# Kernel optimization log

Hardware: AMD Instinct MI355X
Metric: run time of the kernel (lower is better)

## Reference

```python
import jax, jax.numpy as jnp
import numpy as np

H = 1024  # hidden size


def lstm_layer(x, W_ih, W_hh, b_ih, b_hh):
    # x: [B, T, in] -> outputs [B, T, H]; torch gate order (i, f, g, o)
    xg = jnp.einsum('bti,gi->btg', x, W_ih) + (b_ih + b_hh)  # [B, T, 4H]
    xg = jnp.swapaxes(xg, 0, 1)  # [T, B, 4H] for scan over time
    B = x.shape[0]
    h0 = jnp.zeros((B, H), x.dtype)
    c0 = jnp.zeros((B, H), x.dtype)

    def step(carry, xg_t):
        h, c = carry
        g = xg_t + h @ W_hh.T  # [B, 4H]
        i, f, gc, o = jnp.split(g, 4, axis=-1)
        i = jax.nn.sigmoid(i)
        f = jax.nn.sigmoid(f)
        gc = jnp.tanh(gc)
        o = jax.nn.sigmoid(o)
        c = f * c + i * gc
        h = o * jnp.tanh(c)
        return (h, c), h

    (_, _), hs = jax.lax.scan(step, (h0, c0), xg)
    return jnp.swapaxes(hs, 0, 1)  # [B, T, H]


def setup_inputs() -> dict:
    key = jax.random.key(0)
    ks = jax.random.split(key, 11)
    s = 1.0 / np.sqrt(H)  # torch LSTM init scale
    return {
        'x': jax.random.normal(ks[0], (64, 512, 128), jnp.float32),
        'W_ih0': jax.random.normal(ks[1], (4 * H, 128), jnp.float32) * s,
        'W_hh0': jax.random.normal(ks[2], (4 * H, H), jnp.float32) * s,
        'b_ih0': jax.random.normal(ks[3], (4 * H,), jnp.float32) * s,
        'b_hh0': jax.random.normal(ks[4], (4 * H,), jnp.float32) * s,
        'W_ih1': jax.random.normal(ks[5], (4 * H, H), jnp.float32) * s,
        'W_hh1': jax.random.normal(ks[6], (4 * H, H), jnp.float32) * s,
        'b_ih1': jax.random.normal(ks[7], (4 * H,), jnp.float32) * s,
        'b_hh1': jax.random.normal(ks[8], (4 * H,), jnp.float32) * s,
        'fc_w': jax.random.normal(ks[9], (1, H), jnp.float32) * s,
        'fc_b': jax.random.normal(ks[10], (1,), jnp.float32) * s,
    }


def reference(x, W_ih0, W_hh0, b_ih0, b_hh0, W_ih1, W_hh1, b_ih1, b_hh1, fc_w, fc_b):
    h1 = lstm_layer(x, W_ih0, W_hh0, b_ih0, b_hh0)   # [B, T, H]
    h2 = lstm_layer(h1, W_ih1, W_hh1, b_ih1, b_hh1)  # [B, T, H]
    return h2[:, -1, :] @ fc_w.T + fc_b              # [B, 1]
```

## Files before the change

kernel.cpp:

```cpp
#include <hip/hip_runtime.h>
#include <math.h>

#define HDIM 1024
#define BDIM 64
#define TDIM 512
#define KIN  128
#define NBLK 256
#define NTHR 1024
#define FRAME (HDIM * BDIM)

typedef _Float16 f16;
typedef __attribute__((ext_vector_type(2))) _Float16 f16x2;
typedef __attribute__((ext_vector_type(8))) _Float16 f16x8;
typedef __attribute__((ext_vector_type(4))) float f32x4;

#define MFMA16(a, b, c) __builtin_amdgcn_mfma_f32_16x16x32_f16((a), (b), (c), 0, 0, 0)

__device__ __forceinline__ float sigm(float x) { return 1.0f / (1.0f + expf(-x)); }

__device__ __forceinline__ f16x8 ld_cg(const f16* p) {
    f16x8 r;
    asm volatile("global_load_dwordx4 %0, %1, off sc0 sc1"
                 : "=v"(r) : "v"(p) : "memory");
    return r;
}
#define VM_WAIT8(r0, r1, r2, r3, r4, r5, r6, r7)                         \
    asm volatile("s_waitcnt vmcnt(0)"                                    \
                 : "+v"(r0), "+v"(r1), "+v"(r2), "+v"(r3),               \
                   "+v"(r4), "+v"(r5), "+v"(r6), "+v"(r7))

__device__ __forceinline__ void st_cg8(f16* p, uint2 v) {
    asm volatile("global_store_dwordx2 %0, %1, off sc0 sc1"
                 :: "v"(p), "v"(v) : "memory");
}
#define VM_DRAIN() asm volatile("s_waitcnt vmcnt(0)" ::: "memory")

__device__ __forceinline__ void bar_add(unsigned* base, int slot) {
    __hip_atomic_fetch_add(base + slot * 32, 1u, __ATOMIC_RELAXED,
                           __HIP_MEMORY_SCOPE_AGENT);
}
__device__ __forceinline__ void bar_wait(unsigned* base, unsigned target) {
    for (;;) {
        unsigned sum = 0;
        #pragma unroll
        for (int i = 0; i < 8; ++i)
            sum += __hip_atomic_load(base + i * 32, __ATOMIC_RELAXED,
                                     __HIP_MEMORY_SCOPE_AGENT);
        if (sum >= target) break;
        __builtin_amdgcn_s_sleep(1);
    }
}

__global__ void cvt_w(const float* __restrict__ src, f16* __restrict__ dst, int n2) {
    int i = blockIdx.x * blockDim.x + threadIdx.x;
    if (i < n2) {
        float2 a = ((const float2*)src)[i];
        f16x2 o = {(f16)a.x, (f16)a.y};
        ((f16x2*)dst)[i] = o;
    }
}

__global__ void cvt_x(const float* __restrict__ x, f16* __restrict__ xP) {
    int P = blockIdx.x * blockDim.x + threadIdx.x;
    if (P >= TDIM * BDIM * (KIN / 2)) return;
    int kp = P & 63;
    int b  = (P >> 6) & 63;
    int t  = P >> 12;
    float2 v = ((const float2*)x)[((size_t)b * TDIM + t) * (KIN / 2) + kp];
    f16x2 o = {(f16)v.x, (f16)v.y};
    ((f16x2*)xP)[((size_t)t * BDIM + b) * (KIN / 2) + kp] = o;
}

__global__ void __launch_bounds__(NTHR, 4) lstm_fused(
    const f16* __restrict__ xP,
    const f16* __restrict__ Wc0, const f16* __restrict__ Wh0,
    const float* __restrict__ bih0, const float* __restrict__ bhh0,
    const f16* __restrict__ Wc1, const f16* __restrict__ Wh1,
    const float* __restrict__ bih1, const float* __restrict__ bhh1,
    f16* ring1, f16* ring2, unsigned* barA, unsigned* barB) {

    __shared__ float red[32 * 324 + 16];
    __shared__ __align__(16) f16 hbuf1[BDIM * 4];
    __shared__ __align__(16) f16 hbuf2[BDIM * 4];

    const int tid  = threadIdx.x;
    const int lane = tid & 63;
    const int w    = __builtin_amdgcn_readfirstlane(tid >> 6);
    const int bid  = (int)blockIdx.x;
    const int iu4  = __builtin_amdgcn_readfirstlane(bid * 4);
    const int slot = bid & 7;

    const int n    = lane & 15;
    const int quad = lane >> 4;
    const int am   = lane & 15;
    const int wrow = iu4 + (n >> 2) + (n & 3) * HDIM;

    const int oct4 = iu4 >> 3;
    const int coff = iu4 & 7;

    f16x8 B1x;
    f16x8 B1h[2], B2i[2], B2h[2];
    {
        const int kq = quad * 8;
        if (w < 4)
            B1x = *(const f16x8*)(Wc0 + (size_t)wrow * KIN + w * 32 + kq);
        #pragma unroll
        for (int j = 0; j < 2; ++j) {
            const int ks = (2 * w + j) * 32 + kq;
            B1h[j] = *(const f16x8*)(Wh0 + (size_t)wrow * HDIM + ks);
            B2i[j] = *(const f16x8*)(Wc1 + (size_t)wrow * HDIM + ks);
            B2h[j] = *(const f16x8*)(Wh1 + (size_t)wrow * HDIM + ks);
        }
    }

    float bias1[4], bias2[4];
    float c1 = 0.f, c2 = 0.f;
    const int il = w;
    const int m  = lane;
    if (w < 4) {
        const int i = iu4 + il;
        #pragma unroll
        for (int g = 0; g < 4; ++g) {
            bias1[g] = bih0[i + g * HDIM] + bhh0[i + g * HDIM];
            bias2[g] = bih1[i + g * HDIM] + bhh1[i + g * HDIM];
        }
    }

    if (w == 8) {
        uint2 z = {0u, 0u};
        st_cg8(ring1 + FRAME + oct4 * 512 + lane * 8 + coff, z);
        VM_DRAIN();
        if (lane == 0) bar_add(barA, slot);
    }
    if (w == 9) {
        uint2 z = {0u, 0u};
        st_cg8(ring2 + FRAME + oct4 * 512 + lane * 8 + coff, z);
        VM_DRAIN();
        if (lane == 0) bar_add(barB, slot);
    }

    for (int s = 0; s <= TDIM; ++s) {
        const f16* r1p = ring1 + (size_t)((s + 1) & 1) * FRAME;
        const f16* r2p = ring2 + (size_t)(s & 1) * FRAME;

        if (tid == 0) bar_wait(barA, (unsigned)(s + 1) * NBLK);
        __syncthreads();

        f16x8 A1[2][4];
        #pragma unroll
        for (int j = 0; j < 2; ++j) {
            const int oct = (2 * w + j) * 4 + quad;
            #pragma unroll
            for (int mt = 0; mt < 4; ++mt)
                A1[j][mt] = ld_cg(r1p + oct * 512 + (mt * 16 + am) * 8);
        }
        VM_WAIT8(A1[0][0], A1[0][1], A1[0][2], A1[0][3],
                 A1[1][0], A1[1][1], A1[1][2], A1[1][3]);

        f32x4 acc[4], acc2[4];
        #pragma unroll
        for (int mt = 0; mt < 4; ++mt) {
            acc[mt]  = (f32x4){0.f, 0.f, 0.f, 0.f};
            acc2[mt] = (f32x4){0.f, 0.f, 0.f, 0.f};
        }
        #pragma unroll
        for (int j = 0; j < 2; ++j)
            #pragma unroll
            for (int mt = 0; mt < 4; ++mt) {
                acc[mt]  = MFMA16(A1[j][mt], B1h[j], acc[mt]);
                acc2[mt] = MFMA16(A1[j][mt], B2i[j], acc2[mt]);
            }
        if (w < 4) {
            const int ts = (s < TDIM) ? s : (TDIM - 1);
            const f16* xb = xP + (size_t)ts * BDIM * KIN;
            const int kx = w * 32 + quad * 8;
            #pragma unroll
            for (int mt = 0; mt < 4; ++mt) {
                f16x8 ax = *(const f16x8*)(xb + (size_t)(mt * 16 + am) * KIN + kx);
                acc[mt] = MFMA16(ax, B1x, acc[mt]);
            }
        }

        const int p = w & 7;
        if (w < 8) {
            #pragma unroll
            for (int mt = 0; mt < 4; ++mt)
                *(f32x4*)&red[(p * 4 + mt) * 324 + n * 20 + quad * 4] = acc[mt];
        }
        __syncthreads();
        if (w >= 8) {
            #pragma unroll
            for (int mt = 0; mt < 4; ++mt) {
                float* a = &red[(p * 4 + mt) * 324 + n * 20 + quad * 4];
                f32x4 v = *(f32x4*)a;
                *(f32x4*)a = v + acc[mt];
            }
        }
        __syncthreads();

        if (w < 4 && s < TDIM) {
            const int mt = m >> 4, qm = m & 15;
            float g4[4];
            #pragma unroll
            for (int g = 0; g < 4; ++g) {
                float sum = bias1[g];
                #pragma unroll
                for (int pp = 0; pp < 8; ++pp)
                    sum += red[(pp * 4 + mt) * 324 + (il * 4 + g) * 20 + qm];
                g4[g] = sum;
            }
            float ig = sigm(g4[0]), fg = sigm(g4[1]);
            float gg = tanhf(g4[2]), og = sigm(g4[3]);
            c1 = fg * c1 + ig * gg;
            hbuf1[m * 4 + il] = (f16)(og * tanhf(c1));
        }
        if (tid == 64) bar_wait(barB, (unsigned)s * NBLK);
        __syncthreads();

        if (w == 8 && s < TDIM) {
            uint2 v = *(const uint2*)&hbuf1[lane * 4];
            st_cg8(ring1 + (size_t)(s & 1) * FRAME + oct4 * 512 + lane * 8 + coff, v);
            VM_DRAIN();
            if (lane == 0) bar_add(barA, slot);
        }

        f16x8 A2[2][4];
        #pragma unroll
        for (int j = 0; j < 2; ++j) {
            const int oct = (2 * w + j) * 4 + quad;
            #pragma unroll
            for (int mt = 0; mt < 4; ++mt)
                A2[j][mt] = ld_cg(r2p + oct * 512 + (mt * 16 + am) * 8);
        }
        VM_WAIT8(A2[0][0], A2[0][1], A2[0][2], A2[0][3],
                 A2[1][0], A2[1][1], A2[1][2], A2[1][3]);
        #pragma unroll
        for (int j = 0; j < 2; ++j)
            #pragma unroll
            for (int mt = 0; mt < 4; ++mt)
                acc2[mt] = MFMA16(A2[j][mt], B2h[j], acc2[mt]);

        if (w < 8) {
            #pragma unroll
            for (int mt = 0; mt < 4; ++mt)
                *(f32x4*)&red[(p * 4 + mt) * 324 + n * 20 + quad * 4] = acc2[mt];
        }
        __syncthreads();
        if (w >= 8) {
            #pragma unroll
            for (int mt = 0; mt < 4; ++mt) {
                float* a = &red[(p * 4 + mt) * 324 + n * 20 + quad * 4];
                f32x4 v = *(f32x4*)a;
                *(f32x4*)a = v + acc2[mt];
            }
        }
        __syncthreads();

        if (w < 4 && s >= 1) {
            const int mt = m >> 4, qm = m & 15;
            float g4[4];
            #pragma unroll
            for (int g = 0; g < 4; ++g) {
                float sum = bias2[g];
                #pragma unroll
                for (int pp = 0; pp < 8; ++pp)
                    sum += red[(pp * 4 + mt) * 324 + (il * 4 + g) * 20 + qm];
                g4[g] = sum;
            }
            float ig = sigm(g4[0]), fg = sigm(g4[1]);
            float gg = tanhf(g4[2]), og = sigm(g4[3]);
            c2 = fg * c2 + ig * gg;
            hbuf2[m * 4 + il] = (f16)(og * tanhf(c2));
        }
        __syncthreads();

        if (w == 9 && s >= 1) {
            uint2 v = *(const uint2*)&hbuf2[lane * 4];
            st_cg8(ring2 + (size_t)((s + 1) & 1) * FRAME + oct4 * 512 + lane * 8 + coff, v);
            VM_DRAIN();
            if (lane == 0) bar_add(barB, slot);
        }
    }
}

__global__ void fc_kernel(const f16* __restrict__ h2f,
                          const float* __restrict__ fcw,
                          const float* __restrict__ fcb,
                          float* __restrict__ out) {
    __shared__ float red[256];
    const int tid = threadIdx.x;
    const int b = tid >> 2, q = tid & 3;
    float s = 0.f;
    for (int oct = q * 32; oct < (q + 1) * 32; ++oct) {
        f16x8 v = *(const f16x8*)(h2f + oct * 512 + b * 8);
        #pragma unroll
        for (int j = 0; j < 8; ++j)
            s = fmaf((float)v[j], fcw[oct * 8 + j], s);
    }
    red[tid] = s;
    __syncthreads();
    if (q == 0)
        out[b] = red[tid] + red[tid + 1] + red[tid + 2] + red[tid + 3] + fcb[0];
}

extern "C" void kernel_launch(void* const* d_in, const int* in_sizes, int n_in,
                              void* d_out, int out_size, void* d_ws, size_t ws_size,
                              hipStream_t stream) {
    const float* x    = (const float*)d_in[0];
    const float* Wih0 = (const float*)d_in[1];
    const float* Whh0 = (const float*)d_in[2];
    const float* bih0 = (const float*)d_in[3];
    const float* bhh0 = (const float*)d_in[4];
    const float* Wih1 = (const float*)d_in[5];
    const float* Whh1 = (const float*)d_in[6];
    const float* bih1 = (const float*)d_in[7];
    const float* bhh1 = (const float*)d_in[8];
    const float* fcw  = (const float*)d_in[9];
    const float* fcb  = (const float*)d_in[10];
    float* out = (float*)d_out;

    f16* xPd   = (f16*)d_ws;
    f16* Wc0   = xPd + (size_t)TDIM * BDIM * KIN;
    f16* Wh0   = Wc0 + (size_t)4 * HDIM * KIN;
    f16* Wc1   = Wh0 + (size_t)4 * HDIM * HDIM;
    f16* Wh1   = Wc1 + (size_t)4 * HDIM * HDIM;
    f16* ring1 = Wh1 + (size_t)4 * HDIM * HDIM;
    f16* ring2 = ring1 + 2 * FRAME;
    unsigned* barA = (unsigned*)(ring2 + 2 * FRAME);
    unsigned* barB = barA + 1024;

    hipMemsetAsync(barA, 0, 8192, stream);
    {
        int n2 = 4 * HDIM * KIN / 2;
        cvt_w<<<dim3((n2 + 255) / 256), dim3(256), 0, stream>>>(Wih0, Wc0, n2);
        n2 = 4 * HDIM * HDIM / 2;
        cvt_w<<<dim3((n2 + 255) / 256), dim3(256), 0, stream>>>(Whh0, Wh0, n2);
        cvt_w<<<dim3((n2 + 255) / 256), dim3(256), 0, stream>>>(Whh1, Wh1, n2);
        cvt_w<<<dim3((n2 + 255) / 256), dim3(256), 0, stream>>>(Wih1, Wc1, n2);
    }
    {
        int np = TDIM * BDIM * (KIN / 2);
        cvt_x<<<dim3((np + 255) / 256), dim3(256), 0, stream>>>(x, xPd);
    }

    void* args[13];
    args[0]  = (void*)&xPd;
    args[1]  = (void*)&Wc0;
    args[2]  = (void*)&Wh0;
    args[3]  = (void*)&bih0;
    args[4]  = (void*)&bhh0;
    args[5]  = (void*)&Wc1;
    args[6]  = (void*)&Wh1;
    args[7]  = (void*)&bih1;
    args[8]  = (void*)&bhh1;
    args[9]  = (void*)&ring1;
    args[10] = (void*)&ring2;
    args[11] = (void*)&barA;
    args[12] = (void*)&barB;
    hipLaunchCooperativeKernel(reinterpret_cast<void*>(lstm_fused), dim3(NBLK), dim3(NTHR),
                               args, 0, stream);

    fc_kernel<<<dim3(1), dim3(256), 0, stream>>>(ring2 + FRAME, fcw, fcb, out);
}
```

Baseline: 3.225 ms.

## Merge layer barriers into one per step and halve block threads

Cuts the block from 16 to 8 waves, so each wave holds twice the K-slice of weights and h vectors. Both layers' gate pre-activations are now reduced in shared memory in a single pass, and the two grid barriers (one per layer) are replaced by one combined barrier per timestep. Layer 1 and layer 2 cell updates run in parallel on different waves. The goal is fewer grid-wide synchronisations and block syncs per step. In exchange each wave carries more registers and does serial MFMA work, and the second ring load now waits on the same barrier, so the two layers no longer pipeline independently.

After: 3.965 ms. 22.9% more time.

```diff
diff --git a/kernel.cpp b/kernel.cpp
--- a/kernel.cpp
+++ b/kernel.cpp
@@ -6,7 +6,7 @@
 #define TDIM 512
 #define KIN  128
 #define NBLK 256
-#define NTHR 1024
+#define NTHR 512
 #define FRAME (HDIM * BDIM)
 
 typedef _Float16 f16;
@@ -24,10 +24,12 @@
                  : "=v"(r) : "v"(p) : "memory");
     return r;
 }
-#define VM_WAIT8(r0, r1, r2, r3, r4, r5, r6, r7)                         \
+#define VM_WAIT16(a0,a1,a2,a3,a4,a5,a6,a7,b0,b1,b2,b3,b4,b5,b6,b7)       \
     asm volatile("s_waitcnt vmcnt(0)"                                    \
-                 : "+v"(r0), "+v"(r1), "+v"(r2), "+v"(r3),               \
-                   "+v"(r4), "+v"(r5), "+v"(r6), "+v"(r7))
+                 : "+v"(a0), "+v"(a1), "+v"(a2), "+v"(a3),               \
+                   "+v"(a4), "+v"(a5), "+v"(a6), "+v"(a7),               \
+                   "+v"(b0), "+v"(b1), "+v"(b2), "+v"(b3),               \
+                   "+v"(b4), "+v"(b5), "+v"(b6), "+v"(b7))
 
 __device__ __forceinline__ void st_cg8(f16* p, uint2 v) {
     asm volatile("global_store_dwordx2 %0, %1, off sc0 sc1"
@@ -71,13 +73,13 @@
     ((f16x2*)xP)[((size_t)t * BDIM + b) * (KIN / 2) + kp] = o;
 }
 
-__global__ void __launch_bounds__(NTHR, 4) lstm_fused(
+__global__ void __launch_bounds__(NTHR, 2) lstm_fused(
     const f16* __restrict__ xP,
     const f16* __restrict__ Wc0, const f16* __restrict__ Wh0,
     const float* __restrict__ bih0, const float* __restrict__ bhh0,
     const f16* __restrict__ Wc1, const f16* __restrict__ Wh1,
     const float* __restrict__ bih1, const float* __restrict__ bhh1,
-    f16* ring1, f16* ring2, unsigned* barA, unsigned* barB) {
+    f16* ring1, f16* ring2, unsigned* bar) {
 
     __shared__ float red[32 * 324 + 16];
     __shared__ __align__(16) f16 hbuf1[BDIM * 4];
@@ -98,187 +100,166 @@
     const int oct4 = iu4 >> 3;
     const int coff = iu4 & 7;
 
+    f16x8 B1h[4], B2i[4], B2h[4];
     f16x8 B1x;
-    f16x8 B1h[2], B2i[2], B2h[2];
-    {
-        const int kq = quad * 8;
-        if (w < 4)
-            B1x = *(const f16x8*)(Wc0 + (size_t)wrow * KIN + w * 32 + kq);
-        #pragma unroll
-        for (int j = 0; j < 2; ++j) {
-            const int ks = (2 * w + j) * 32 + kq;
-            B1h[j] = *(const f16x8*)(Wh0 + (size_t)wrow * HDIM + ks);
-            B2i[j] = *(const f16x8*)(Wc1 + (size_t)wrow * HDIM + ks);
-            B2h[j] = *(const f16x8*)(Wh1 + (size_t)wrow * HDIM + ks);
-        }
-    }
-
-    float bias1[4], bias2[4];
-    float c1 = 0.f, c2 = 0.f;
-    const int il = w;
+    #pragma unroll
+    for (int j = 0; j < 4; ++j) {
+        const int ks = w * 128 + j * 32 + quad * 8;
+        B1h[j] = *(const f16x8*)(Wh0 + (size_t)wrow * HDIM + ks);
+        B2i[j] = *(const f16x8*)(Wc1 + (size_t)wrow * HDIM + ks);
+        B2h[j] = *(const f16x8*)(Wh1 + (size_t)wrow * HDIM + ks);
+    }
+    if (w < 4)
+        B1x = *(const f16x8*)(Wc0 + (size_t)wrow * KIN + w * 32 + quad * 8);
+
+    const int il = (w < 4) ? w : (w - 4);
     const int m  = lane;
-    if (w < 4) {
-        const int i = iu4 + il;
-        #pragma unroll
-        for (int g = 0; g < 4; ++g) {
-            bias1[g] = bih0[i + g * HDIM] + bhh0[i + g * HDIM];
-            bias2[g] = bih1[i + g * HDIM] + bhh1[i + g * HDIM];
-        }
-    }
-
-    if (w == 8) {
-        uint2 z = {0u, 0u};
-        st_cg8(ring1 + FRAME + oct4 * 512 + lane * 8 + coff, z);
+    const int icol = iu4 + il;
+    float bias[4];
+    float c = 0.f;
+    if (w < 8) {
+        const float* bi = (w < 4) ? bih0 : bih1;
+        const float* bh = (w < 4) ? bhh0 : bhh1;
+        #pragma unroll
+        for (int g = 0; g < 4; ++g)
+            bias[g] = bi[icol + g * HDIM] + bh[icol + g * HDIM];
+    }
+
+    if (w == 0) {
+        st_cg8(ring1 + FRAME + oct4 * 512 + lane * 8 + coff, (uint2){0u, 0u});
         VM_DRAIN();
-        if (lane == 0) bar_add(barA, slot);
-    }
-    if (w == 9) {
-        uint2 z = {0u, 0u};
-        st_cg8(ring2 + FRAME + oct4 * 512 + lane * 8 + coff, z);
+        if (lane == 0) bar_add(bar, slot);
+    }
+    if (w == 1) {
+        st_cg8(ring2 + FRAME + oct4 * 512 + lane * 8 + coff, (uint2){0u, 0u});
         VM_DRAIN();
-        if (lane == 0) bar_add(barB, slot);
+        if (lane == 0) bar_add(bar, slot);
     }
 
     for (int s = 0; s <= TDIM; ++s) {
+        if (tid == 0) bar_wait(bar, (unsigned)(s + 1) * (2 * NBLK));
+        __syncthreads();
+
         const f16* r1p = ring1 + (size_t)((s + 1) & 1) * FRAME;
         const f16* r2p = ring2 + (size_t)(s & 1) * FRAME;
 
-        if (tid == 0) bar_wait(barA, (unsigned)(s + 1) * NBLK);
-        __syncthreads();
-
-        f16x8 A1[2][4];
-        #pragma unroll
-        for (int j = 0; j < 2; ++j) {
-            const int oct = (2 * w + j) * 4 + quad;
+        f16x8 A1[4][4];
+        #pragma unroll
+        for (int j = 0; j < 4; ++j) {
+            const int oct = (w * 4 + j) * 4 + quad;
             #pragma unroll
             for (int mt = 0; mt < 4; ++mt)
                 A1[j][mt] = ld_cg(r1p + oct * 512 + (mt * 16 + am) * 8);
         }
-        VM_WAIT8(A1[0][0], A1[0][1], A1[0][2], A1[0][3],
-                 A1[1][0], A1[1][1], A1[1][2], A1[1][3]);
-
-        f32x4 acc[4], acc2[4];
-        #pragma unroll
-        for (int mt = 0; mt < 4; ++mt) {
-            acc[mt]  = (f32x4){0.f, 0.f, 0.f, 0.f};
-            acc2[mt] = (f32x4){0.f, 0.f, 0.f, 0.f};
-        }
-        #pragma unroll
-        for (int j = 0; j < 2; ++j)
-            #pragma unroll
-            for (int mt = 0; mt < 4; ++mt) {
-                acc[mt]  = MFMA16(A1[j][mt], B1h[j], acc[mt]);
-                acc2[mt] = MFMA16(A1[j][mt], B2i[j], acc2[mt]);
-            }
+        f16x8 ax[4];
         if (w < 4) {
             const int ts = (s < TDIM) ? s : (TDIM - 1);
             const f16* xb = xP + (size_t)ts * BDIM * KIN;
             const int kx = w * 32 + quad * 8;
             #pragma unroll
+            for (int mt = 0; mt < 4; ++mt)
+                ax[mt] = *(const f16x8*)(xb + (size_t)(mt * 16 + am) * KIN + kx);
+        }
+        VM_WAIT16(A1[0][0], A1[0][1], A1[0][2], A1[0][3],
+                  A1[1][0], A1[1][1], A1[1][2], A1[1][3],
+                  A1[2][0], A1[2][1], A1[2][2], A1[2][3],
+                  A1[3][0], A1[3][1], A1[3][2], A1[3][3]);
+
+        f32x4 acc[4], acc2[4];
+        #pragma unroll
+        for (int mt = 0; mt < 4; ++mt) {
+            acc[mt]  = (f32x4){0.f, 0.f, 0.f, 0.f};
+            acc2[mt] = (f32x4){0.f, 0.f, 0.f, 0.f};
+        }
+        #pragma unroll
+        for (int j = 0; j < 4; ++j)
+            #pragma unroll
             for (int mt = 0; mt < 4; ++mt) {
-                f16x8 ax = *(const f16x8*)(xb + (size_t)(mt * 16 + am) * KIN + kx);
-                acc[mt] = MFMA16(ax, B1x, acc[mt]);
-            }
-        }
-
-        const int p = w & 7;
-        if (w < 8) {
-            #pragma unroll
-            for (int mt = 0; mt < 4; ++mt)
+                acc[mt]  = MFMA16(A1[j][mt], B1h[j], acc[mt]);
+                acc2[mt] = MFMA16(A1[j][mt], B2i[j], acc2[mt]);
+            }
+        if (w < 4) {
+            #pragma unroll
+            for (int mt = 0; mt < 4; ++mt)
+                acc[mt] = MFMA16(ax[mt], B1x, acc[mt]);
+        }
+
+        f16x8 A2[4][4];
+        #pragma unroll
+        for (int j = 0; j < 4; ++j) {
+            const int oct = (w * 4 + j) * 4 + quad;
+            #pragma unroll
+            for (int mt = 0; mt < 4; ++mt)
+                A2[j][mt] = ld_cg(r2p + oct * 512 + (mt * 16 + am) * 8);
+        }
+        VM_WAIT16(A2[0][0], A2[0][1], A2[0][2], A2[0][3],
+                  A2[1][0], A2[1][1], A2[1][2], A2[1][3],
+                  A2[2][0], A2[2][1], A2[2][2], A2[2][3],
+                  A2[3][0], A2[3][1], A2[3][2], A2[3][3]);
+        #pragma unroll
+        for (int j = 0; j < 4; ++j)
+            #pragma unroll
+            for (int mt = 0; mt < 4; ++mt)
+                acc2[mt] = MFMA16(A2[j][mt], B2h[j], acc2[mt]);
+
+        const int p = w & 3;
+        if (w < 4) {
+            #pragma unroll
+            for (int mt = 0; mt < 4; ++mt) {
                 *(f32x4*)&red[(p * 4 + mt) * 324 + n * 20 + quad * 4] = acc[mt];
+                *(f32x4*)&red[(16 + p * 4 + mt) * 324 + n * 20 + quad * 4] = acc2[mt];
+            }
         }
         __syncthreads();
-        if (w >= 8) {
+        if (w >= 4) {
             #pragma unroll
             for (int mt = 0; mt < 4; ++mt) {
-                float* a = &red[(p * 4 + mt) * 324 + n * 20 + quad * 4];
-                f32x4 v = *(f32x4*)a;
-                *(f32x4*)a = v + acc[mt];
+                float* a1 = &red[(p * 4 + mt) * 324 + n * 20 + quad * 4];
+                float* a2 = &red[(16 + p * 4 + mt) * 324 + n * 20 + quad * 4];
+                f32x4 v1 = *(f32x4*)a1;
+                f32x4 v2 = *(f32x4*)a2;
+                *(f32x4*)a1 = v1 + acc[mt];
+                *(f32x4*)a2 = v2 + acc2[mt];
             }
         }
         __syncthreads();
 
-        if (w < 4 && s < TDIM) {
-            const int mt = m >> 4, qm = m & 15;
+        if ((w < 4 && s < TDIM) || (w >= 4 && s >= 1)) {
+            const int base = (w < 4) ? 0 : 16 * 324;
+            const int mtm = m >> 4, qm = m & 15;
             float g4[4];
             #pragma unroll
             for (int g = 0; g < 4; ++g) {
-                float sum = bias1[g];
+                float sum = bias[g];
                 #pragma unroll
-                for (int pp = 0; pp < 8; ++pp)
-                    sum += red[(pp * 4 + mt) * 324 + (il * 4 + g) * 20 + qm];
+                for (int pp = 0; pp < 4; ++pp)
+                    sum += red[base + (pp * 4 + mtm) * 324 + (il * 4 + g) * 20 + qm];
                 g4[g] = sum;
             }
             float ig = sigm(g4[0]), fg = sigm(g4[1]);
             float gg = tanhf(g4[2]), og = sigm(g4[3]);
-            c1 = fg * c1 + ig * gg;
-            hbuf1[m * 4 + il] = (f16)(og * tanhf(c1));
-        }
-        if (tid == 64) bar_wait(barB, (unsigned)s * NBLK);
+            c = fg * c + ig * gg;
+            float h = og * tanhf(c);
+            if (w < 4) hbuf1[m * 4 + il] = (f16)h;
+            else       hbuf2[m * 4 + il] = (f16)h;
+        }
         __syncthreads();
 
-        if (w == 8 && s < TDIM) {
-            uint2 v = *(const uint2*)&hbuf1[lane * 4];
-            st_cg8(ring1 + (size_t)(s & 1) * FRAME + oct4 * 512 + lane * 8 + coff, v);
-            VM_DRAIN();
-            if (lane == 0) bar_add(barA, slot);
-        }
-
-        f16x8 A2[2][4];
-        #pragma unroll
-        for (int j = 0; j < 2; ++j) {
-            const int oct = (2 * w + j) * 4 + quad;
-            #pragma unroll
-            for (int mt = 0; mt < 4; ++mt)
-                A2[j][mt] = ld_cg(r2p + oct * 512 + (mt * 16 + am) * 8);
-        }
-        VM_WAIT8(A2[0][0], A2[0][1], A2[0][2], A2[0][3],
-                 A2[1][0], A2[1][1], A2[1][2], A2[1][3]);
-        #pragma unroll
-        for (int j = 0; j < 2; ++j)
-            #pragma unroll
-            for (int mt = 0; mt < 4; ++mt)
-                acc2[mt] = MFMA16(A2[j][mt], B2h[j], acc2[mt]);
-
-        if (w < 8) {
-            #pragma unroll
-            for (int mt = 0; mt < 4; ++mt)
-                *(f32x4*)&red[(p * 4 + mt) * 324 + n * 20 + quad * 4] = acc2[mt];
-        }
-        __syncthreads();
-        if (w >= 8) {
-            #pragma unroll
-            for (int mt = 0; mt < 4; ++mt) {
-                float* a = &red[(p * 4 + mt) * 324 + n * 20 + quad * 4];
-                f32x4 v = *(f32x4*)a;
-                *(f32x4*)a = v + acc2[mt];
-            }
-        }
-        __syncthreads();
-
-        if (w < 4 && s >= 1) {
-            const int mt = m >> 4, qm = m & 15;
-            float g4[4];
-            #pragma unroll
-            for (int g = 0; g < 4; ++g) {
-                float sum = bias2[g];
-                #pragma unroll
-                for (int pp = 0; pp < 8; ++pp)
-                    sum += red[(pp * 4 + mt) * 324 + (il * 4 + g) * 20 + qm];
-                g4[g] = sum;
-            }
-            float ig = sigm(g4[0]), fg = sigm(g4[1]);
-            float gg = tanhf(g4[2]), og = sigm(g4[3]);
-            c2 = fg * c2 + ig * gg;
-            hbuf2[m * 4 + il] = (f16)(og * tanhf(c2));
-        }
-        __syncthreads();
-
-        if (w == 9 && s >= 1) {
-            uint2 v = *(const uint2*)&hbuf2[lane * 4];
-            st_cg8(ring2 + (size_t)((s + 1) & 1) * FRAME + oct4 * 512 + lane * 8 + coff, v);
-            VM_DRAIN();
-            if (lane == 0) bar_add(barB, slot);
+        if (w == 0) {
+            if (s < TDIM) {
+                uint2 v = *(const uint2*)&hbuf1[lane * 4];
+                st_cg8(ring1 + (size_t)(s & 1) * FRAME + oct4 * 512 + lane * 8 + coff, v);
+                VM_DRAIN();
+            }
+            if (lane == 0) bar_add(bar, slot);
+        }
+        if (w == 1) {
+            if (s >= 1) {
+                uint2 v = *(const uint2*)&hbuf2[lane * 4];
+                st_cg8(ring2 + (size_t)((s + 1) & 1) * FRAME + oct4 * 512 + lane * 8 + coff, v);
+                VM_DRAIN();
+            }
+            if (lane == 0) bar_add(bar, slot);
         }
     }
 }
@@ -326,10 +307,9 @@
     f16* Wh1   = Wc1 + (size_t)4 * HDIM * HDIM;
     f16* ring1 = Wh1 + (size_t)4 * HDIM * HDIM;
     f16* ring2 = ring1 + 2 * FRAME;
-    unsigned* barA = (unsigned*)(ring2 + 2 * FRAME);
-    unsigned* barB = barA + 1024;
-
-    hipMemsetAsync(barA, 0, 8192, stream);
+    unsigned* bar = (unsigned*)(ring2 + 2 * FRAME);
+
+    hipMemsetAsync(bar, 0, 4096, stream);
     {
         int n2 = 4 * HDIM * KIN / 2;
         cvt_w<<<dim3((n2 + 255) / 256), dim3(256), 0, stream>>>(Wih0, Wc0, n2);
@@ -343,7 +323,7 @@
         cvt_x<<<dim3((np + 255) / 256), dim3(256), 0, stream>>>(x, xPd);
     }
 
-    void* args[13];
+    void* args[12];
     args[0]  = (void*)&xPd;
     args[1]  = (void*)&Wc0;
     args[2]  = (void*)&Wh0;
@@ -355,8 +335,7 @@
     args[8]  = (void*)&bhh1;
     args[9]  = (void*)&ring1;
     args[10] = (void*)&ring2;
-    args[11] = (void*)&barA;
-    args[12] = (void*)&barB;
+    args[11] = (void*)&bar;
     hipLaunchCooperativeKernel(reinterpret_cast<void*>(lstm_fused), dim3(NBLK), dim3(NTHR),
                                args, 0, stream);
 
```

## Split blocks between LSTM layers and pipeline them through four-deep ring buffers

Applied to the files above, without the earlier changes.

Assigns blocks 0-127 to layer 1 and blocks 128-255 to layer 2, with each block owning 8 hidden units instead of 4 for both layers. The two layers now run as a producer-consumer pipeline synchronised through separate barriers and 4-slot ring buffers, so each block waits only on its own layer's barrier plus a lagged cross-layer dependency instead of serialising both layers within one step. Stores widen to 16-byte writes. In exchange, each block does twice the MFMA work per step and adds more intra-block reduction stages. The cross-layer barrier offsets must be right to avoid races.

New measurement: 3.912 ms. 21.3% more time.

```diff
diff --git a/kernel.cpp b/kernel.cpp
--- a/kernel.cpp
+++ b/kernel.cpp
@@ -8,11 +8,13 @@
 #define NBLK 256
 #define NTHR 1024
 #define FRAME (HDIM * BDIM)
+#define LHALF 128
 
 typedef _Float16 f16;
 typedef __attribute__((ext_vector_type(2))) _Float16 f16x2;
 typedef __attribute__((ext_vector_type(8))) _Float16 f16x8;
 typedef __attribute__((ext_vector_type(4))) float f32x4;
+typedef __attribute__((ext_vector_type(4))) unsigned u32x4;
 
 #define MFMA16(a, b, c) __builtin_amdgcn_mfma_f32_16x16x32_f16((a), (b), (c), 0, 0, 0)
 
@@ -29,8 +31,8 @@
                  : "+v"(r0), "+v"(r1), "+v"(r2), "+v"(r3),               \
                    "+v"(r4), "+v"(r5), "+v"(r6), "+v"(r7))
 
-__device__ __forceinline__ void st_cg8(f16* p, uint2 v) {
-    asm volatile("global_store_dwordx2 %0, %1, off sc0 sc1"
+__device__ __forceinline__ void st_cg16(f16* p, u32x4 v) {
+    asm volatile("global_store_dwordx4 %0, %1, off sc0 sc1"
                  :: "v"(p), "v"(v) : "memory");
 }
 #define VM_DRAIN() asm volatile("s_waitcnt vmcnt(0)" ::: "memory")
@@ -80,205 +82,305 @@
     f16* ring1, f16* ring2, unsigned* barA, unsigned* barB) {
 
     __shared__ float red[32 * 324 + 16];
-    __shared__ __align__(16) f16 hbuf1[BDIM * 4];
-    __shared__ __align__(16) f16 hbuf2[BDIM * 4];
+    __shared__ __align__(16) f16 hbuf[BDIM * 8];
 
     const int tid  = threadIdx.x;
     const int lane = tid & 63;
     const int w    = __builtin_amdgcn_readfirstlane(tid >> 6);
     const int bid  = (int)blockIdx.x;
-    const int iu4  = __builtin_amdgcn_readfirstlane(bid * 4);
+    const int lay2 = bid >> 7;
+    const int oct  = __builtin_amdgcn_readfirstlane(bid & 127);
+    const int iu8  = oct * 8;
     const int slot = bid & 7;
 
     const int n    = lane & 15;
     const int quad = lane >> 4;
     const int am   = lane & 15;
-    const int wrow = iu4 + (n >> 2) + (n & 3) * HDIM;
-
-    const int oct4 = iu4 >> 3;
-    const int coff = iu4 & 7;
-
-    f16x8 B1x;
-    f16x8 B1h[2], B2i[2], B2h[2];
+    const int m    = lane;
+
+    int wr0 = iu8 + (n >> 2) + (n & 3) * HDIM;
+    int wr1 = wr0 + 4;
+
+    const int il = w & 7;
+    const int icol = iu8 + il;
+    float bias[4];
+    float c = 0.f;
     {
-        const int kq = quad * 8;
-        if (w < 4)
-            B1x = *(const f16x8*)(Wc0 + (size_t)wrow * KIN + w * 32 + kq);
+        const float* bi = lay2 ? bih1 : bih0;
+        const float* bh = lay2 ? bhh1 : bhh0;
+        #pragma unroll
+        for (int g = 0; g < 4; ++g)
+            bias[g] = bi[icol + g * HDIM] + bh[icol + g * HDIM];
+    }
+
+    const int p = w & 3;
+
+    if (!lay2) {
+        f16x8 B1h[2][2], B1x[2];
         #pragma unroll
         for (int j = 0; j < 2; ++j) {
-            const int ks = (2 * w + j) * 32 + kq;
-            B1h[j] = *(const f16x8*)(Wh0 + (size_t)wrow * HDIM + ks);
-            B2i[j] = *(const f16x8*)(Wc1 + (size_t)wrow * HDIM + ks);
-            B2h[j] = *(const f16x8*)(Wh1 + (size_t)wrow * HDIM + ks);
-        }
-    }
-
-    float bias1[4], bias2[4];
-    float c1 = 0.f, c2 = 0.f;
-    const int il = w;
-    const int m  = lane;
-    if (w < 4) {
-        const int i = iu4 + il;
-        #pragma unroll
-        for (int g = 0; g < 4; ++g) {
-            bias1[g] = bih0[i + g * HDIM] + bhh0[i + g * HDIM];
-            bias2[g] = bih1[i + g * HDIM] + bhh1[i + g * HDIM];
-        }
-    }
-
-    if (w == 8) {
-        uint2 z = {0u, 0u};
-        st_cg8(ring1 + FRAME + oct4 * 512 + lane * 8 + coff, z);
-        VM_DRAIN();
-        if (lane == 0) bar_add(barA, slot);
-    }
-    if (w == 9) {
-        uint2 z = {0u, 0u};
-        st_cg8(ring2 + FRAME + oct4 * 512 + lane * 8 + coff, z);
-        VM_DRAIN();
-        if (lane == 0) bar_add(barB, slot);
-    }
-
-    for (int s = 0; s <= TDIM; ++s) {
-        const f16* r1p = ring1 + (size_t)((s + 1) & 1) * FRAME;
-        const f16* r2p = ring2 + (size_t)(s & 1) * FRAME;
-
-        if (tid == 0) bar_wait(barA, (unsigned)(s + 1) * NBLK);
-        __syncthreads();
-
-        f16x8 A1[2][4];
+            const int ks = (2 * w + j) * 32 + quad * 8;
+            B1h[j][0] = *(const f16x8*)(Wh0 + (size_t)wr0 * HDIM + ks);
+            B1h[j][1] = *(const f16x8*)(Wh0 + (size_t)wr1 * HDIM + ks);
+        }
+        if (w < 4) {
+            const int kx = w * 32 + quad * 8;
+            B1x[0] = *(const f16x8*)(Wc0 + (size_t)wr0 * KIN + kx);
+            B1x[1] = *(const f16x8*)(Wc0 + (size_t)wr1 * KIN + kx);
+        }
+        if (w == 8) {
+            st_cg16(ring1 + 3 * (size_t)FRAME + oct * 512 + lane * 8,
+                    (u32x4){0u, 0u, 0u, 0u});
+            VM_DRAIN();
+            if (lane == 0) bar_add(barA, slot);
+        }
+
+        for (int t = 0; t < TDIM; ++t) {
+            if (tid == 0)  bar_wait(barA, (unsigned)(t + 1) * LHALF);
+            if (tid == 64 && t >= 4) bar_wait(barB, (unsigned)(t - 2) * LHALF);
+            __syncthreads();
+
+            const f16* r1p = ring1 + (size_t)((t + 3) & 3) * FRAME;
+            f16x8 A1[2][4];
+            #pragma unroll
+            for (int j = 0; j < 2; ++j) {
+                const int ok = (2 * w + j) * 4 + quad;
+                #pragma unroll
+                for (int mt = 0; mt < 4; ++mt)
+                    A1[j][mt] = ld_cg(r1p + ok * 512 + (mt * 16 + am) * 8);
+            }
+            f16x8 ax[4];
+            if (w < 4) {
+                const f16* xb = xP + (size_t)t * BDIM * KIN;
+                const int kx = w * 32 + quad * 8;
+                #pragma unroll
+                for (int mt = 0; mt < 4; ++mt)
+                    ax[mt] = *(const f16x8*)(xb + (size_t)(mt * 16 + am) * KIN + kx);
+            }
+            VM_WAIT8(A1[0][0], A1[0][1], A1[0][2], A1[0][3],
+                     A1[1][0], A1[1][1], A1[1][2], A1[1][3]);
+
+            f32x4 acc[2][4];
+            #pragma unroll
+            for (int nt = 0; nt < 2; ++nt)
+                #pragma unroll
+                for (int mt = 0; mt < 4; ++mt)
+                    acc[nt][mt] = (f32x4){0.f, 0.f, 0.f, 0.f};
+            #pragma unroll
+            for (int j = 0; j < 2; ++j)
+                #pragma unroll
+                for (int nt = 0; nt < 2; ++nt)
+                    #pragma unroll
+                    for (int mt = 0; mt < 4; ++mt)
+                        acc[nt][mt] = MFMA16(A1[j][mt], B1h[j][nt], acc[nt][mt]);
+            if (w < 4) {
+                #pragma unroll
+                for (int nt = 0; nt < 2; ++nt)
+                    #pragma unroll
+                    for (int mt = 0; mt < 4; ++mt)
+                        acc[nt][mt] = MFMA16(ax[mt], B1x[nt], acc[nt][mt]);
+            }
+
+            if (w < 4) {
+                #pragma unroll
+                for (int nt = 0; nt < 2; ++nt)
+                    #pragma unroll
+                    for (int mt = 0; mt < 4; ++mt)
+                        *(f32x4*)&red[((nt * 4 + p) * 4 + mt) * 324 + n * 20 + quad * 4] = acc[nt][mt];
+            }
+            __syncthreads();
+            if (w >= 4 && w < 8) {
+                #pragma unroll
+                for (int nt = 0; nt < 2; ++nt)
+                    #pragma unroll
+                    for (int mt = 0; mt < 4; ++mt) {
+                        float* a = &red[((nt * 4 + p) * 4 + mt) * 324 + n * 20 + quad * 4];
+                        *(f32x4*)a = *(f32x4*)a + acc[nt][mt];
+                    }
+            }
+            __syncthreads();
+            if (w >= 8 && w < 12) {
+                #pragma unroll
+                for (int nt = 0; nt < 2; ++nt)
+                    #pragma unroll
+                    for (int mt = 0; mt < 4; ++mt) {
+                        float* a = &red[((nt * 4 + p) * 4 + mt) * 324 + n * 20 + quad * 4];
+                        *(f32x4*)a = *(f32x4*)a + acc[nt][mt];
+                    }
+            }
+            __syncthreads();
+            if (w >= 12) {
+                #pragma unroll
+                for (int nt = 0; nt < 2; ++nt)
+                    #pragma unroll
+                    for (int mt = 0; mt < 4; ++mt) {
+                        float* a = &red[((nt * 4 + p) * 4 + mt) * 324 + n * 20 + quad * 4];
+                        *(f32x4*)a = *(f32x4*)a + acc[nt][mt];
+                    }
+            }
+            __syncthreads();
+
+            if (w < 8) {
+                const int ntl = il >> 2, cl = il & 3;
+                const int mtm = m >> 4, qm = m & 15;
+                float g4[4];
+                #pragma unroll
+                for (int g = 0; g < 4; ++g) {
+                    float sum = bias[g];
+                    #pragma unroll
+                    for (int pp = 0; pp < 4; ++pp)
+                        sum += red[((ntl * 4 + pp) * 4 + mtm) * 324 + (cl * 4 + g) * 20 + qm];
+                    g4[g] = sum;
+                }
+                float ig = sigm(g4[0]), fg = sigm(g4[1]);
+                float gg = tanhf(g4[2]), og = sigm(g4[3]);
+                c = fg * c + ig * gg;
+                hbuf[m * 8 + il] = (f16)(og * tanhf(c));
+            }
+            __syncthreads();
+
+            if (w == 8) {
+                u32x4 v = *(const u32x4*)&hbuf[lane * 8];
+                st_cg16(ring1 + (size_t)(t & 3) * FRAME + oct * 512 + lane * 8, v);
+                VM_DRAIN();
+                if (lane == 0) bar_add(barA, slot);
+            }
+        }
+    } else {
+        f16x8 B2i[2][2], B2h[2][2];
         #pragma unroll
         for (int j = 0; j < 2; ++j) {
-            const int oct = (2 * w + j) * 4 + quad;
-            #pragma unroll
-            for (int mt = 0; mt < 4; ++mt)
-                A1[j][mt] = ld_cg(r1p + oct * 512 + (mt * 16 + am) * 8);
-        }
-        VM_WAIT8(A1[0][0], A1[0][1], A1[0][2], A1[0][3],
-                 A1[1][0], A1[1][1], A1[1][2], A1[1][3]);
-
-        f32x4 acc[4], acc2[4];
-        #pragma unroll
-        for (int mt = 0; mt < 4; ++mt) {
-            acc[mt]  = (f32x4){0.f, 0.f, 0.f, 0.f};
-            acc2[mt] = (f32x4){0.f, 0.f, 0.f, 0.f};
-        }
-        #pragma unroll
-        for (int j = 0; j < 2; ++j)
-            #pragma unroll
-            for (int mt = 0; mt < 4; ++mt) {
-                acc[mt]  = MFMA16(A1[j][mt], B1h[j], acc[mt]);
-                acc2[mt] = MFMA16(A1[j][mt], B2i[j], acc2[mt]);
-            }
-        if (w < 4) {
-            const int ts = (s < TDIM) ? s : (TDIM - 1);
-            const f16* xb = xP + (size_t)ts * BDIM * KIN;
-            const int kx = w * 32 + quad * 8;
-            #pragma unroll
-            for (int mt = 0; mt < 4; ++mt) {
-                f16x8 ax = *(const f16x8*)(xb + (size_t)(mt * 16 + am) * KIN + kx);
-                acc[mt] = MFMA16(ax, B1x, acc[mt]);
-            }
-        }
-
-        const int p = w & 7;
-        if (w < 8) {
-            #pragma unroll
-            for (int mt = 0; mt < 4; ++mt)
-                *(f32x4*)&red[(p * 4 + mt) * 324 + n * 20 + quad * 4] = acc[mt];
-        }
-        __syncthreads();
-        if (w >= 8) {
-            #pragma unroll
-            for (int mt = 0; mt < 4; ++mt) {
-                float* a = &red[(p * 4 + mt) * 324 + n * 20 + quad * 4];
-                f32x4 v = *(f32x4*)a;
-                *(f32x4*)a = v + acc[mt];
-            }
-        }
-        __syncthreads();
-
-        if (w < 4 && s < TDIM) {
-            const int mt = m >> 4, qm = m & 15;
-            float g4[4];
-            #pragma unroll
-            for (int g = 0; g < 4; ++g) {
-                float sum = bias1[g];
-                #pragma unroll
-                for (int pp = 0; pp < 8; ++pp)
-                    sum += red[(pp * 4 + mt) * 324 + (il * 4 + g) * 20 + qm];
-                g4[g] = sum;
-            }
-            float ig = sigm(g4[0]), fg = sigm(g4[1]);
-            float gg = tanhf(g4[2]), og = sigm(g4[3]);
-            c1 = fg * c1 + ig * gg;
-            hbuf1[m * 4 + il] = (f16)(og * tanhf(c1));
-        }
-        if (tid == 64) bar_wait(barB, (unsigned)s * NBLK);
-        __syncthreads();
-
-        if (w == 8 && s < TDIM) {
-            uint2 v = *(const uint2*)&hbuf1[lane * 4];
-            st_cg8(ring1 + (size_t)(s & 1) * FRAME + oct4 * 512 + lane * 8 + coff, v);
-            VM_DRAIN();
-            if (lane == 0) bar_add(barA, slot);
-        }
-
-        f16x8 A2[2][4];
-        #pragma unroll
-        for (int j = 0; j < 2; ++j) {
-            const int oct = (2 * w + j) * 4 + quad;
-            #pragma unroll
-            for (int mt = 0; mt < 4; ++mt)
-                A2[j][mt] = ld_cg(r2p + oct * 512 + (mt * 16 + am) * 8);
-        }
-        VM_WAIT8(A2[0][0], A2[0][1], A2[0][2], A2[0][3],
-                 A2[1][0], A2[1][1], A2[1][2], A2[1][3]);
-        #pragma unroll
-        for (int j = 0; j < 2; ++j)
-            #pragma unroll
-            for (int mt = 0; mt < 4; ++mt)
-                acc2[mt] = MFMA16(A2[j][mt], B2h[j], acc2[mt]);
-
-        if (w < 8) {
-            #pragma unroll
-            for (int mt = 0; mt < 4; ++mt)
-                *(f32x4*)&red[(p * 4 + mt) * 324 + n * 20 + quad * 4] = acc2[mt];
-        }
-        __syncthreads();
-        if (w >= 8) {
-            #pragma unroll
-            for (int mt = 0; mt < 4; ++mt) {
-                float* a = &red[(p * 4 + mt) * 324 + n * 20 + quad * 4];
-                f32x4 v = *(f32x4*)a;
-                *(f32x4*)a = v + acc2[mt];
-            }
-        }
-        __syncthreads();
-
-        if (w < 4 && s >= 1) {
-            const int mt = m >> 4, qm = m & 15;
-            float g4[4];
-            #pragma unroll
-            for (int g = 0; g < 4; ++g) {
-                float sum = bias2[g];
-                #pragma unroll
-                for (int pp = 0; pp < 8; ++pp)
-                    sum += red[(pp * 4 + mt) * 324 + (il * 4 + g) * 20 + qm];
-                g4[g] = sum;
-            }
-            float ig = sigm(g4[0]), fg = sigm(g4[1]);
-            float gg = tanhf(g4[2]), og = sigm(g4[3]);
-            c2 = fg * c2 + ig * gg;
-            hbuf2[m * 4 + il] = (f16)(og * tanhf(c2));
-        }
-        __syncthreads();
-
-        if (w == 9 && s >= 1) {
-            uint2 v = *(const uint2*)&hbuf2[lane * 4];
-            st_cg8(ring2 + (size_t)((s + 1) & 1) * FRAME + oct4 * 512 + lane * 8 + coff, v);
+            const int ks = (2 * w + j) * 32 + quad * 8;
+            B2i[j][0] = *(const f16x8*)(Wc1 + (size_t)wr0 * HDIM + ks);
+            B2i[j][1] = *(const f16x8*)(Wc1 + (size_t)wr1 * HDIM + ks);
+            B2h[j][0] = *(const f16x8*)(Wh1 + (size_t)wr0 * HDIM + ks);
+            B2h[j][1] = *(const f16x8*)(Wh1 + (size_t)wr1 * HDIM + ks);
+        }
+        if (w == 8) {
+            st_cg16(ring2 + 3 * (size_t)FRAME + oct * 512 + lane * 8,
+                    (u32x4){0u, 0u, 0u, 0u});
             VM_DRAIN();
             if (lane == 0) bar_add(barB, slot);
+        }
+
+        for (int u = 0; u < TDIM; ++u) {
+            if (tid == 0)  bar_wait(barB, (unsigned)(u + 1) * LHALF);
+            if (tid == 64) bar_wait(barA, (unsigned)(u + 2) * LHALF);
+            __syncthreads();
+
+            const f16* r2p = ring2 + (size_t)((u + 3) & 3) * FRAME;
+            const f16* r1p = ring1 + (size_t)(u & 3) * FRAME;
+
+            f32x4 acc2[2][4];
+            #pragma unroll
+            for (int nt = 0; nt < 2; ++nt)
+                #pragma unroll
+                for (int mt = 0; mt < 4; ++mt)
+                    acc2[nt][mt] = (f32x4){0.f, 0.f, 0.f, 0.f};
+
+            {
+                f16x8 A[2][4];
+                #pragma unroll
+                for (int j = 0; j < 2; ++j) {
+                    const int ok = (2 * w + j) * 4 + quad;
+                    #pragma unroll
+                    for (int mt = 0; mt < 4; ++mt)
+                        A[j][mt] = ld_cg(r2p + ok * 512 + (mt * 16 + am) * 8);
+                }
+                VM_WAIT8(A[0][0], A[0][1], A[0][2], A[0][3],
+                         A[1][0], A[1][1], A[1][2], A[1][3]);
+                #pragma unroll
+                for (int j = 0; j < 2; ++j)
+                    #pragma unroll
+                    for (int nt = 0; nt < 2; ++nt)
+                        #pragma unroll
+                        for (int mt = 0; mt < 4; ++mt)
+                            acc2[nt][mt] = MFMA16(A[j][mt], B2h[j][nt], acc2[nt][mt]);
+            }
+            {
+                f16x8 A[2][4];
+                #pragma unroll
+                for (int j = 0; j < 2; ++j) {
+                    const int ok = (2 * w + j) * 4 + quad;
+                    #pragma unroll
+                    for (int mt = 0; mt < 4; ++mt)
+                        A[j][mt] = ld_cg(r1p + ok * 512 + (mt * 16 + am) * 8);
+                }
+                VM_WAIT8(A[0][0], A[0][1], A[0][2], A[0][3],
+                         A[1][0], A[1][1], A[1][2], A[1][3]);
+                #pragma unroll
+                for (int j = 0; j < 2; ++j)
+                    #pragma unroll
+                    for (int nt = 0; nt < 2; ++nt)
+                        #pragma unroll
+                        for (int mt = 0; mt < 4; ++mt)
+                            acc2[nt][mt] = MFMA16(A[j][mt], B2i[j][nt], acc2[nt][mt]);
+            }
+
+            if (w < 4) {
+                #pragma unroll
+                for (int nt = 0; nt < 2; ++nt)
+                    #pragma unroll
+                    for (int mt = 0; mt < 4; ++mt)
+                        *(f32x4*)&red[((nt * 4 + p) * 4 + mt) * 324 + n * 20 + quad * 4] = acc2[nt][mt];
+            }
+            __syncthreads();
+            if (w >= 4 && w < 8) {
+                #pragma unroll
+                for (int nt = 0; nt < 2; ++nt)
+                    #pragma unroll
+                    for (int mt = 0; mt < 4; ++mt) {
+                        float* a = &red[((nt * 4 + p) * 4 + mt) * 324 + n * 20 + quad * 4];
+                        *(f32x4*)a = *(f32x4*)a + acc2[nt][mt];
+                    }
+            }
+            __syncthreads();
+            if (w >= 8 && w < 12) {
+                #pragma unroll
+                for (int nt = 0; nt < 2; ++nt)
+                    #pragma unroll
+                    for (int mt = 0; mt < 4; ++mt) {
+                        float* a = &red[((nt * 4 + p) * 4 + mt) * 324 + n * 20 + quad * 4];
+                        *(f32x4*)a = *(f32x4*)a + acc2[nt][mt];
+                    }
+            }
+            __syncthreads();
+            if (w >= 12) {
+                #pragma unroll
+                for (int nt = 0; nt < 2; ++nt)
+                    #pragma unroll
+                    for (int mt = 0; mt < 4; ++mt) {
+                        float* a = &red[((nt * 4 + p) * 4 + mt) * 324 + n * 20 + quad * 4];
+                        *(f32x4*)a = *(f32x4*)a + acc2[nt][mt];
+                    }
+            }
+            __syncthreads();
+
+            if (w < 8) {
+                const int ntl = il >> 2, cl = il & 3;
+                const int mtm = m >> 4, qm = m & 15;
+                float g4[4];
+                #pragma unroll
+                for (int g = 0; g < 4; ++g) {
+                    float sum = bias[g];
+                    #pragma unroll
+                    for (int pp = 0; pp < 4; ++pp)
+                        sum += red[((ntl * 4 + pp) * 4 + mtm) * 324 + (cl * 4 + g) * 20 + qm];
+                    g4[g] = sum;
+                }
+                float ig = sigm(g4[0]), fg = sigm(g4[1]);
+                float gg = tanhf(g4[2]), og = sigm(g4[3]);
+                c = fg * c + ig * gg;
+                hbuf[m * 8 + il] = (f16)(og * tanhf(c));
+            }
+            __syncthreads();
+
+            if (w == 8) {
+                u32x4 v = *(const u32x4*)&hbuf[lane * 8];
+                st_cg16(ring2 + (size_t)(u & 3) * FRAME + oct * 512 + lane * 8, v);
+                VM_DRAIN();
+                if (lane == 0) bar_add(barB, slot);
+            }
         }
     }
 }
@@ -325,8 +427,8 @@
     f16* Wc1   = Wh0 + (size_t)4 * HDIM * HDIM;
     f16* Wh1   = Wc1 + (size_t)4 * HDIM * HDIM;
     f16* ring1 = Wh1 + (size_t)4 * HDIM * HDIM;
-    f16* ring2 = ring1 + 2 * FRAME;
-    unsigned* barA = (unsigned*)(ring2 + 2 * FRAME);
+    f16* ring2 = ring1 + 4 * (size_t)FRAME;
+    unsigned* barA = (unsigned*)(ring2 + 4 * (size_t)FRAME);
     unsigned* barB = barA + 1024;
 
     hipMemsetAsync(barA, 0, 8192, stream);
@@ -360,5 +462,5 @@
     hipLaunchCooperativeKernel(reinterpret_cast<void*>(lstm_fused), dim3(NBLK), dim3(NTHR),
                                args, 0, stream);
 
-    fc_kernel<<<dim3(1), dim3(256), 0, stream>>>(ring2 + FRAME, fcw, fcb, out);
-}
+    fc_kernel<<<dim3(1), dim3(256), 0, stream>>>(ring2 + 3 * (size_t)FRAME, fcw, fcb, out);
+}
```
